# Optimization experiments

Measured on AMD Instinct MI355X. Metric: run time of the kernel, lower is better.

Reference implementation:

```python
import jax, jax.numpy as jnp
import numpy as np

B, T, D = 128, 512, 400
N_VALS, N_ACTS = 1024, 128

def setup_inputs() -> dict:
    key = jax.random.key(0)
    ks = jax.random.split(key, 7)
    H_utt = jax.random.normal(ks[0], (B, T, D), dtype=jnp.float32)
    c_utt = jax.random.normal(ks[1], (B, D), dtype=jnp.float32)
    C_acts = jax.random.normal(ks[2], (B, N_ACTS, D), dtype=jnp.float32)
    C_vals = jax.random.normal(ks[3], (N_VALS, 1, D), dtype=jnp.float32)
    W_score = jax.random.normal(ks[4], (1, D), dtype=jnp.float32) * (1.0 / np.sqrt(D))
    b_score = jnp.zeros((1,), dtype=jnp.float32)
    lens = jax.random.randint(ks[5], (B,), T // 2, T + 1, dtype=jnp.int64 if jax.config.read('jax_enable_x64') else jnp.int32)
    lens = lens.at[0].set(T)  # ensure max(lens) == T so masking matches torch semantics
    return {"H_utt": H_utt, "c_utt": c_utt, "C_acts": C_acts, "C_vals": C_vals,
            "W_score": W_score, "b_score": b_score, "utterance_len": lens}

def reference(H_utt, c_utt, C_acts, C_vals, W_score, b_score, utterance_len):
    vals = C_vals[:, 0, :]                                   # [V, D]
    # --- y_utts: default attention of each value vector over utterance states ---
    scores = jnp.einsum('btd,vd->bvt', H_utt, vals)          # mul+sum scoring
    mask = jnp.arange(T)[None, :] < utterance_len[:, None]   # [B, T]
    scores = jnp.where(mask[:, None, :], scores, -jnp.inf)
    probs = jax.nn.softmax(scores, axis=-1)                  # [B, V, T]
    q_utts = jnp.einsum('bvt,btd->bvd', probs, H_utt)        # weighted sum contexts
    y_utts = jnp.einsum('bvd,d->bv', q_utts, W_score[0]) + b_score[0]  # utt_scorer
    # --- y_acts: attention of c_utt over per-example act vectors, then score vs vals ---
    s2 = jnp.einsum('bad,bd->ba', C_acts, c_utt)
    p2 = jax.nn.softmax(s2, axis=-1)
    q_acts = jnp.einsum('ba,bad->bd', p2, C_acts)            # [B, D]
    y_acts = q_acts @ vals.T                                 # [B, V]
    return (y_utts, y_acts)
```

## Files before the change

### kernel.cpp

```cpp
#include <hip/hip_runtime.h>
#include <hip/hip_bf16.h>

#define B_  128
#define T_  512
#define D_  400
#define NV  1024
#define NA  128

#define LDH  424
#define NT   32
#define MV   128
#define MAIN_BLOCKS 1024

typedef __bf16 bf16_t;
typedef bf16_t bf16x8 __attribute__((ext_vector_type(8)));
typedef bf16_t bf16x4 __attribute__((ext_vector_type(4)));
typedef float  floatx4 __attribute__((ext_vector_type(4)));

__device__ inline void async_copy16(const void* g, void* l) {
    __builtin_amdgcn_global_load_lds(
        (const __attribute__((address_space(1))) unsigned int*)g,
        (__attribute__((address_space(3))) unsigned int*)l, 16, 0, 0);
}

__device__ inline float dot4(float4 a, float4 b) {
    return a.x * b.x + a.y * b.y + a.z * b.z + a.w * b.w;
}

__global__ __launch_bounds__(256) void prep_kernel(const float* __restrict__ H,
                                                   const float* __restrict__ W,
                                                   const float* __restrict__ Ca,
                                                   const float* __restrict__ cu,
                                                   float* __restrict__ hw,
                                                   bf16_t* __restrict__ Hbf,
                                                   float* __restrict__ s2) {
    int wave = threadIdx.x >> 6;
    int lane = threadIdx.x & 63;
    if (blockIdx.x < B_ * T_ / 4) {
        long row = (long)blockIdx.x * 4 + wave;
        const float* h = H + row * D_;
        bf16_t* orow = Hbf + row * (long)LDH;
        float acc = 0.f;
        if (lane < 50) {
            const float4* p  = (const float4*)(h + lane * 8);
            const float4* wp = (const float4*)(W + lane * 8);
            float4 x = p[0], y = p[1];
            acc = dot4(x, wp[0]) + dot4(y, wp[1]);
            bf16x8 f;
            f[0] = (bf16_t)x.x; f[1] = (bf16_t)x.y; f[2] = (bf16_t)x.z; f[3] = (bf16_t)x.w;
            f[4] = (bf16_t)y.x; f[5] = (bf16_t)y.y; f[6] = (bf16_t)y.z; f[7] = (bf16_t)y.w;
            *(bf16x8*)(orow + lane * 8) = f;
        } else if (lane < 53) {
            bf16x8 z;
#pragma unroll
            for (int j = 0; j < 8; ++j) z[j] = (bf16_t)0.0f;
            *(bf16x8*)(orow + 400 + (lane - 50) * 8) = z;
        }
#pragma unroll
        for (int off = 1; off < 64; off <<= 1) acc += __shfl_xor(acc, off, 64);
        if (lane == 0) hw[row] = acc;
    } else {
        long row = (long)(blockIdx.x - B_ * T_ / 4) * 4 + wave;
        int b = (int)(row >> 7);
        const float4* a4 = (const float4*)(Ca + row * (long)D_);
        const float4* c4 = (const float4*)(cu + (long)b * D_);
        float acc = dot4(a4[lane], c4[lane]);
        if (lane < 36) acc += dot4(a4[lane + 64], c4[lane + 64]);
#pragma unroll
        for (int off = 1; off < 64; off <<= 1) acc += __shfl_xor(acc, off, 64);
        if (lane == 0) s2[row] = acc;
    }
}

__global__ __launch_bounds__(256) void prep_nb_kernel(const float* __restrict__ H,
                                                      const float* __restrict__ W,
                                                      const float* __restrict__ Ca,
                                                      const float* __restrict__ cu,
                                                      float* __restrict__ hw,
                                                      float* __restrict__ s2) {
    int wave = threadIdx.x >> 6;
    int lane = threadIdx.x & 63;
    if (blockIdx.x < B_ * T_ / 4) {
        long row = (long)blockIdx.x * 4 + wave;
        const float* h = H + row * D_;
        float acc = 0.f;
        for (int k = lane; k < D_; k += 64) acc += h[k] * W[k];
#pragma unroll
        for (int off = 1; off < 64; off <<= 1) acc += __shfl_xor(acc, off, 64);
        if (lane == 0) hw[row] = acc;
    } else {
        long row = (long)(blockIdx.x - B_ * T_ / 4) * 4 + wave;
        int b = (int)(row >> 7);
        const float4* a4 = (const float4*)(Ca + row * (long)D_);
        const float4* c4 = (const float4*)(cu + (long)b * D_);
        float acc = dot4(a4[lane], c4[lane]);
        if (lane < 36) acc += dot4(a4[lane + 64], c4[lane + 64]);
#pragma unroll
        for (int off = 1; off < 64; off <<= 1) acc += __shfl_xor(acc, off, 64);
        if (lane == 0) s2[row] = acc;
    }
}

__global__ __launch_bounds__(256) void qacts_kernel(const float* __restrict__ s2,
                                                    const float* __restrict__ Ca,
                                                    float* __restrict__ q_ws) {
    __shared__ float p_lds[NA];
    __shared__ float red[8];
    __shared__ __align__(16) float4 part[100];
    int b = blockIdx.x;
    int tid = threadIdx.x, wave = tid >> 6, lane = tid & 63;

    float s = (tid < NA) ? s2[(long)b * NA + tid] : -3.0e38f;
    float m = s;
#pragma unroll
    for (int off = 1; off < 64; off <<= 1) m = fmaxf(m, __shfl_xor(m, off, 64));
    if (lane == 0) red[wave] = m;
    __syncthreads();
    m = fmaxf(red[0], red[1]);
    float e = (tid < NA) ? __expf(s - m) : 0.f;
    float sum = e;
#pragma unroll
    for (int off = 1; off < 64; off <<= 1) sum += __shfl_xor(sum, off, 64);
    if (lane == 0) red[4 + wave] = sum;
    __syncthreads();
    float S = red[4] + red[5];
    if (tid < NA) p_lds[tid] = e / S;
    __syncthreads();

    int c4 = tid % 100;
    int half = tid / 100;
    float4 acc0 = {0.f, 0.f, 0.f, 0.f};
    if (tid < 200) {
        const float4* Cb4 = (const float4*)(Ca + (size_t)b * NA * D_);
        float4 acc1 = {0.f, 0.f, 0.f, 0.f};
        int a0 = half * 64;
#pragma unroll 4
        for (int a = 0; a < 64; a += 2) {
            float p0 = p_lds[a0 + a], p1 = p_lds[a0 + a + 1];
            float4 x0 = Cb4[(size_t)(a0 + a) * 100 + c4];
            float4 x1 = Cb4[(size_t)(a0 + a + 1) * 100 + c4];
            acc0.x += p0 * x0.x; acc0.y += p0 * x0.y; acc0.z += p0 * x0.z; acc0.w += p0 * x0.w;
            acc1.x += p1 * x1.x; acc1.y += p1 * x1.y; acc1.z += p1 * x1.z; acc1.w += p1 * x1.w;
        }
        acc0.x += acc1.x; acc0.y += acc1.y; acc0.z += acc1.z; acc0.w += acc1.w;
        if (half == 1) part[c4] = acc0;
    }
    __syncthreads();
    if (tid < 100) {
        float4 o = part[c4];
        o.x += acc0.x; o.y += acc0.y; o.z += acc0.z; o.w += acc0.w;
        ((float4*)(q_ws + (size_t)b * D_))[c4] = o;
    }
}

template<int PRE>
__global__ __launch_bounds__(256, 3) void main_kernel(const float* __restrict__ H,
                                                      const bf16_t* __restrict__ Hbf,
                                                      const float* __restrict__ Cv,
                                                      const float* __restrict__ hw,
                                                      const float* __restrict__ bs,
                                                      const int* __restrict__ lens,
                                                      const float* __restrict__ q_ws,
                                                      float* __restrict__ out) {
    __shared__ bf16_t h_lds[NT * LDH + 256];
    __shared__ float hw_lds[NT];

    int tid = threadIdx.x;
    int wave = tid >> 6, lane = tid & 63;

    if (blockIdx.x >= MAIN_BLOCKS) {
        long grp = (long)(blockIdx.x - MAIN_BLOCKS) * 4 + wave;
        int b = (int)(grp >> 8);
        int v0 = (int)(grp & 255) * 4;
        const float4* q4 = (const float4*)(q_ws + (size_t)b * D_);
        float4 qa = q4[lane];
        float4 qb = (lane < 36) ? q4[lane + 64] : make_float4(0.f, 0.f, 0.f, 0.f);
        float acc[4];
#pragma unroll
        for (int r = 0; r < 4; ++r) {
            const float4* v4 = (const float4*)(Cv + (size_t)(v0 + r) * D_);
            acc[r] = dot4(v4[lane], qa);
            if (lane < 36) acc[r] += dot4(v4[lane + 64], qb);
        }
#pragma unroll
        for (int off = 1; off < 64; off <<= 1) {
#pragma unroll
            for (int r = 0; r < 4; ++r) acc[r] += __shfl_xor(acc[r], off, 64);
        }
        if (lane == 0) {
            float4 o = make_float4(acc[0], acc[1], acc[2], acc[3]);
            *(float4*)(out + (size_t)B_ * NV + (size_t)b * NV + v0) = o;
        }
        return;
    }

    int i = blockIdx.x;
    int xcd = i & 7, vc = (i >> 3) & 7, bb = i >> 6;
    int b = xcd + 8 * bb;
    int vbase = vc * MV;

    int lrow = lane & 15, quad = lane >> 4;
    int len = lens[b];
    float b0 = bs[0];

    if (!PRE) {
        for (int idx = tid; idx < NT * (LDH - D_); idx += 256) {
            int r = idx / (LDH - D_), c = idx % (LDH - D_);
            h_lds[r * LDH + D_ + c] = (bf16_t)0.0f;
        }
    }

    bf16x8 afrag[2][13];
#pragma unroll
    for (int set = 0; set < 2; ++set) {
        const float* vrow = Cv + (size_t)(vbase + wave * 32 + set * 16 + lrow) * D_;
#pragma unroll
        for (int kk = 0; kk < 13; ++kk) {
            int k0 = kk * 32 + quad * 8;
            bf16x8 f;
            if (k0 >= D_) {
#pragma unroll
                for (int j = 0; j < 8; ++j) f[j] = (bf16_t)0.0f;
            } else {
                const float4* p = (const float4*)(vrow + k0);
                float4 x = p[0], y = p[1];
                f[0] = (bf16_t)x.x; f[1] = (bf16_t)x.y;
                f[2] = (bf16_t)x.z; f[3] = (bf16_t)x.w;
                f[4] = (bf16_t)y.x; f[5] = (bf16_t)y.y;
                f[6] = (bf16_t)y.z; f[7] = (bf16_t)y.w;
            }
            afrag[set][kk] = f;
        }
    }

    float m_s = -3.0e38f;
    float l_s[2][4], a_s[2][4];
#pragma unroll
    for (int set = 0; set < 2; ++set)
#pragma unroll
        for (int r = 0; r < 4; ++r) { l_s[set][r] = 0.f; a_s[set][r] = 0.f; }

    int ntiles = (len + NT - 1) / NT;
    const float* Hb = H + (size_t)b * T_ * D_;
    const bf16_t* Hbfb = Hbf + (size_t)b * T_ * LDH;

    for (int tt = 0; tt < ntiles; ++tt) {
        int t0 = tt * NT;
        __syncthreads();
        if (PRE) {
            const char* gt = (const char*)(Hbfb + (size_t)t0 * LDH);
            char* lt = (char*)h_lds;
#pragma unroll 1
            for (int c = wave; c < 27; c += 4)
                async_copy16(gt + c * 1024 + lane * 16, lt + c * 1024 + lane * 16);
        } else {
            for (int idx = tid; idx < NT * (D_ / 4); idx += 256) {
                int r = idx / (D_ / 4), c4 = idx % (D_ / 4);
                float4 x = *(const float4*)(Hb + (size_t)(t0 + r) * D_ + c4 * 4);
                bf16x4 f;
                f[0] = (bf16_t)x.x; f[1] = (bf16_t)x.y;
                f[2] = (bf16_t)x.z; f[3] = (bf16_t)x.w;
                *(bf16x4*)(&h_lds[r * LDH + c4 * 4]) = f;
            }
        }
        if (tid < NT) hw_lds[tid] = hw[(size_t)b * T_ + t0 + tid];
        __syncthreads();

        floatx4 c[2][2];
        floatx4 zero4 = {0.f, 0.f, 0.f, 0.f};
#pragma unroll
        for (int set = 0; set < 2; ++set)
#pragma unroll
            for (int s = 0; s < 2; ++s) c[set][s] = zero4;

#pragma unroll
        for (int kk = 0; kk < 13; ++kk) {
            int koff = kk * 32 + quad * 8;
#pragma unroll
            for (int s = 0; s < 2; ++s) {
                bf16x8 bfr = *(const bf16x8*)(&h_lds[(s * 16 + lrow) * LDH + koff]);
                c[0][s] = __builtin_amdgcn_mfma_f32_16x16x32_bf16(afrag[0][kk], bfr, c[0][s], 0, 0, 0);
                c[1][s] = __builtin_amdgcn_mfma_f32_16x16x32_bf16(afrag[1][kk], bfr, c[1][s], 0, 0, 0);
            }
        }

        if (t0 + NT > len) {
#pragma unroll
            for (int s = 0; s < 2; ++s) {
                int t = t0 + s * 16 + lrow;
                if (t >= len) {
#pragma unroll
                    for (int set = 0; set < 2; ++set) {
                        c[set][s][0] = -3.0e38f; c[set][s][1] = -3.0e38f;
                        c[set][s][2] = -3.0e38f; c[set][s][3] = -3.0e38f;
                    }
                }
            }
        }

        float hw0 = hw_lds[lrow], hw1 = hw_lds[16 + lrow];

        float cm = fmaxf(fmaxf(fmaxf(c[0][0][0], c[0][0][1]), fmaxf(c[0][0][2], c[0][0][3])),
                         fmaxf(fmaxf(c[0][1][0], c[0][1][1]), fmaxf(c[0][1][2], c[0][1][3])));
        cm = fmaxf(cm,
             fmaxf(fmaxf(fmaxf(c[1][0][0], c[1][0][1]), fmaxf(c[1][0][2], c[1][0][3])),
                   fmaxf(fmaxf(c[1][1][0], c[1][1][1]), fmaxf(c[1][1][2], c[1][1][3]))));
        float mn = fmaxf(m_s, cm);
        float alpha = __expf(m_s - mn);
        m_s = mn;
#pragma unroll
        for (int set = 0; set < 2; ++set)
#pragma unroll
            for (int r = 0; r < 4; ++r) {
                float p0 = __expf(c[set][0][r] - mn);
                float p1 = __expf(c[set][1][r] - mn);
                l_s[set][r] = l_s[set][r] * alpha + (p0 + p1);
                a_s[set][r] = a_s[set][r] * alpha + (p0 * hw0 + p1 * hw1);
            }
    }

#pragma unroll
    for (int set = 0; set < 2; ++set)
#pragma unroll
        for (int r = 0; r < 4; ++r) {
            float m = m_s, l = l_s[set][r], a = a_s[set][r];
#pragma unroll
            for (int off = 1; off < 16; off <<= 1) {
                float mo = __shfl_xor(m, off, 64);
                float lo = __shfl_xor(l, off, 64);
                float ao = __shfl_xor(a, off, 64);
                float mx = fmaxf(m, mo);
                float f1 = __expf(m - mx), f2 = __expf(mo - mx);
                l = l * f1 + lo * f2;
                a = a * f1 + ao * f2;
                m = mx;
            }
            if (lrow == 0) {
                int v = vbase + wave * 32 + set * 16 + quad * 4 + r;
                out[(size_t)b * NV + v] = a / l + b0;
            }
        }
}

extern "C" void kernel_launch(void* const* d_in, const int* in_sizes, int n_in,
                              void* d_out, int out_size, void* d_ws, size_t ws_size,
                              hipStream_t stream) {
    const float* H    = (const float*)d_in[0];
    const float* cu   = (const float*)d_in[1];
    const float* Ca   = (const float*)d_in[2];
    const float* Cv   = (const float*)d_in[3];
    const float* W    = (const float*)d_in[4];
    const float* bs   = (const float*)d_in[5];
    const int*   lens = (const int*)d_in[6];
    float* out = (float*)d_out;

    float*  hw   = (float*)d_ws;
    float*  q_ws = hw + (size_t)B_ * T_;
    float*  s2   = q_ws + (size_t)B_ * D_;
    bf16_t* Hbf  = (bf16_t*)(s2 + (size_t)B_ * NA);

    size_t need = ((size_t)B_ * T_ + (size_t)B_ * D_ + (size_t)B_ * NA) * sizeof(float)
                + (size_t)B_ * T_ * LDH * sizeof(bf16_t)
                + 4096;
    bool pre = (ws_size >= need);

    int prep_blocks = B_ * T_ / 4 + B_ * NA / 4;
    if (pre) {
        prep_kernel<<<dim3(prep_blocks), dim3(256), 0, stream>>>(H, W, Ca, cu, hw, Hbf, s2);
    } else {
        prep_nb_kernel<<<dim3(prep_blocks), dim3(256), 0, stream>>>(H, W, Ca, cu, hw, s2);
    }
    qacts_kernel<<<dim3(B_), dim3(256), 0, stream>>>(s2, Ca, q_ws);
    int fused_blocks = MAIN_BLOCKS + B_ * NV / 16;
    if (pre) {
        main_kernel<1><<<dim3(fused_blocks), dim3(256), 0, stream>>>(H, Hbf, Cv, hw, bs, lens, q_ws, out);
    } else {
        main_kernel<0><<<dim3(fused_blocks), dim3(256), 0, stream>>>(H, Hbf, Cv, hw, bs, lens, q_ws, out);
    }
}
```

Measured before the change: 288.5 us.

## Pre-swizzle H into MFMA fragment layout and stream from registers, dropping LDS

The prep kernel now writes H as bf16 in 16-row tiles already arranged in the MFMA B-fragment order, so each lane loads its fragment straight from global memory with no LDS staging and no block barriers. The main kernel gives each wave 64 values (four 16-wide sets) and double-buffers tile fragments in registers, with half as many blocks at occupancy 1. Padded tiles past the length are skipped at 16-row granularity. This removes the LDS round trip and syncthreads, but register pressure is higher, occupancy is lower, and every wave rereads the H tiles from global/L2.

```diff
diff --git a/kernel.cpp b/kernel.cpp
--- a/kernel.cpp
+++ b/kernel.cpp
@@ -7,21 +7,17 @@
 #define NV  1024
 #define NA  128
 
+#define TILE_BYTES 13312
+#define MAIN_BLOCKS 512
+
 #define LDH  424
 #define NT   32
-#define MV   128
-#define MAIN_BLOCKS 1024
+#define FB_MAIN_BLOCKS 1024
 
 typedef __bf16 bf16_t;
 typedef bf16_t bf16x8 __attribute__((ext_vector_type(8)));
 typedef bf16_t bf16x4 __attribute__((ext_vector_type(4)));
 typedef float  floatx4 __attribute__((ext_vector_type(4)));
-
-__device__ inline void async_copy16(const void* g, void* l) {
-    __builtin_amdgcn_global_load_lds(
-        (const __attribute__((address_space(1))) unsigned int*)g,
-        (__attribute__((address_space(3))) unsigned int*)l, 16, 0, 0);
-}
 
 __device__ inline float dot4(float4 a, float4 b) {
     return a.x * b.x + a.y * b.y + a.z * b.z + a.w * b.w;
@@ -32,64 +28,40 @@
                                                    const float* __restrict__ Ca,
                                                    const float* __restrict__ cu,
                                                    float* __restrict__ hw,
-                                                   bf16_t* __restrict__ Hbf,
+                                                   bf16_t* __restrict__ Hf,
                                                    float* __restrict__ s2) {
     int wave = threadIdx.x >> 6;
     int lane = threadIdx.x & 63;
-    if (blockIdx.x < B_ * T_ / 4) {
-        long row = (long)blockIdx.x * 4 + wave;
-        const float* h = H + row * D_;
-        bf16_t* orow = Hbf + row * (long)LDH;
+    if (blockIdx.x < 1024) {
+        int tile = blockIdx.x * 4 + wave;
+        int b = tile >> 5, ti = tile & 31;
+        int lrow = lane & 15, quad = lane >> 4;
+        const float* hrow = H + ((size_t)b * T_ + ti * 16 + lrow) * D_;
+        char* fdst = (char*)Hf + (size_t)tile * TILE_BYTES + lane * 16;
         float acc = 0.f;
-        if (lane < 50) {
-            const float4* p  = (const float4*)(h + lane * 8);
-            const float4* wp = (const float4*)(W + lane * 8);
-            float4 x = p[0], y = p[1];
-            acc = dot4(x, wp[0]) + dot4(y, wp[1]);
+#pragma unroll
+        for (int kk = 0; kk < 13; ++kk) {
+            int k0 = kk * 32 + quad * 8;
             bf16x8 f;
-            f[0] = (bf16_t)x.x; f[1] = (bf16_t)x.y; f[2] = (bf16_t)x.z; f[3] = (bf16_t)x.w;
-            f[4] = (bf16_t)y.x; f[5] = (bf16_t)y.y; f[6] = (bf16_t)y.z; f[7] = (bf16_t)y.w;
-            *(bf16x8*)(orow + lane * 8) = f;
-        } else if (lane < 53) {
-            bf16x8 z;
-#pragma unroll
-            for (int j = 0; j < 8; ++j) z[j] = (bf16_t)0.0f;
-            *(bf16x8*)(orow + 400 + (lane - 50) * 8) = z;
-        }
-#pragma unroll
-        for (int off = 1; off < 64; off <<= 1) acc += __shfl_xor(acc, off, 64);
-        if (lane == 0) hw[row] = acc;
+            if (k0 < D_) {
+                float4 x = *(const float4*)(hrow + k0);
+                float4 y = *(const float4*)(hrow + k0 + 4);
+                float4 wx = *(const float4*)(W + k0);
+                float4 wy = *(const float4*)(W + k0 + 4);
+                acc += dot4(x, wx) + dot4(y, wy);
+                f[0] = (bf16_t)x.x; f[1] = (bf16_t)x.y; f[2] = (bf16_t)x.z; f[3] = (bf16_t)x.w;
+                f[4] = (bf16_t)y.x; f[5] = (bf16_t)y.y; f[6] = (bf16_t)y.z; f[7] = (bf16_t)y.w;
+            } else {
+#pragma unroll
+                for (int j = 0; j < 8; ++j) f[j] = (bf16_t)0.0f;
+            }
+            *(bf16x8*)(fdst + kk * 1024) = f;
+        }
+        acc += __shfl_xor(acc, 16, 64);
+        acc += __shfl_xor(acc, 32, 64);
+        if (lane < 16) hw[b * T_ + ti * 16 + lane] = acc;
     } else {
-        long row = (long)(blockIdx.x - B_ * T_ / 4) * 4 + wave;
-        int b = (int)(row >> 7);
-        const float4* a4 = (const float4*)(Ca + row * (long)D_);
-        const float4* c4 = (const float4*)(cu + (long)b * D_);
-        float acc = dot4(a4[lane], c4[lane]);
-        if (lane < 36) acc += dot4(a4[lane + 64], c4[lane + 64]);
-#pragma unroll
-        for (int off = 1; off < 64; off <<= 1) acc += __shfl_xor(acc, off, 64);
-        if (lane == 0) s2[row] = acc;
-    }
-}
-
-__global__ __launch_bounds__(256) void prep_nb_kernel(const float* __restrict__ H,
-                                                      const float* __restrict__ W,
-                                                      const float* __restrict__ Ca,
-                                                      const float* __restrict__ cu,
-                                                      float* __restrict__ hw,
-                                                      float* __restrict__ s2) {
-    int wave = threadIdx.x >> 6;
-    int lane = threadIdx.x & 63;
-    if (blockIdx.x < B_ * T_ / 4) {
-        long row = (long)blockIdx.x * 4 + wave;
-        const float* h = H + row * D_;
-        float acc = 0.f;
-        for (int k = lane; k < D_; k += 64) acc += h[k] * W[k];
-#pragma unroll
-        for (int off = 1; off < 64; off <<= 1) acc += __shfl_xor(acc, off, 64);
-        if (lane == 0) hw[row] = acc;
-    } else {
-        long row = (long)(blockIdx.x - B_ * T_ / 4) * 4 + wave;
+        long row = (long)(blockIdx.x - 1024) * 4 + wave;
         int b = (int)(row >> 7);
         const float4* a4 = (const float4*)(Ca + row * (long)D_);
         const float4* c4 = (const float4*)(cu + (long)b * D_);
@@ -153,18 +125,48 @@
     }
 }
 
-template<int PRE>
-__global__ __launch_bounds__(256, 3) void main_kernel(const float* __restrict__ H,
-                                                      const bf16_t* __restrict__ Hbf,
+#define LDTILE(BUF, TI)                                                        \
+    _Pragma("unroll") for (int kk = 0; kk < 13; ++kk)                          \
+        BUF[kk] = *(const bf16x8*)(fb + (size_t)(TI) * TILE_BYTES + kk * 1024);
+
+#define COMPUTE(BUF, TI)                                                       \
+    do {                                                                       \
+        floatx4 c_[4];                                                         \
+        _Pragma("unroll") for (int s_ = 0; s_ < 4; ++s_) c_[s_] = zero4;       \
+        _Pragma("unroll") for (int kk = 0; kk < 13; ++kk) {                    \
+            bf16x8 bb_ = BUF[kk];                                              \
+            _Pragma("unroll") for (int s_ = 0; s_ < 4; ++s_)                   \
+                c_[s_] = __builtin_amdgcn_mfma_f32_16x16x32_bf16(              \
+                    afrag[s_][kk], bb_, c_[s_], 0, 0, 0);                      \
+        }                                                                      \
+        int t_ = (TI) * 16 + lrow;                                             \
+        float hwv_ = hwb[t_];                                                  \
+        bool ok_ = t_ < len;                                                   \
+        float cm_ = -3.0e38f;                                                  \
+        _Pragma("unroll") for (int s_ = 0; s_ < 4; ++s_)                       \
+            _Pragma("unroll") for (int r_ = 0; r_ < 4; ++r_) {                 \
+                float v_ = ok_ ? c_[s_][r_] : -3.0e38f;                        \
+                c_[s_][r_] = v_;                                               \
+                cm_ = fmaxf(cm_, v_);                                          \
+            }                                                                  \
+        float mn_ = fmaxf(m_s, cm_);                                           \
+        float alpha_ = __expf(m_s - mn_);                                      \
+        m_s = mn_;                                                             \
+        _Pragma("unroll") for (int s_ = 0; s_ < 4; ++s_)                       \
+            _Pragma("unroll") for (int r_ = 0; r_ < 4; ++r_) {                 \
+                float p_ = __expf(c_[s_][r_] - mn_);                           \
+                l_s[s_][r_] = l_s[s_][r_] * alpha_ + p_;                       \
+                a_s[s_][r_] = a_s[s_][r_] * alpha_ + p_ * hwv_;                \
+            }                                                                  \
+    } while (0)
+
+__global__ __launch_bounds__(256, 1) void main_kernel(const bf16_t* __restrict__ Hf,
                                                       const float* __restrict__ Cv,
                                                       const float* __restrict__ hw,
                                                       const float* __restrict__ bs,
                                                       const int* __restrict__ lens,
                                                       const float* __restrict__ q_ws,
                                                       float* __restrict__ out) {
-    __shared__ bf16_t h_lds[NT * LDH + 256];
-    __shared__ float hw_lds[NT];
-
     int tid = threadIdx.x;
     int wave = tid >> 6, lane = tid & 63;
 
@@ -195,25 +197,18 @@
     }
 
     int i = blockIdx.x;
-    int xcd = i & 7, vc = (i >> 3) & 7, bb = i >> 6;
+    int xcd = i & 7, vc = (i >> 3) & 3, bb = i >> 5;
     int b = xcd + 8 * bb;
-    int vbase = vc * MV;
+    int vbase = vc * 256 + wave * 64;
 
     int lrow = lane & 15, quad = lane >> 4;
     int len = lens[b];
     float b0 = bs[0];
 
-    if (!PRE) {
-        for (int idx = tid; idx < NT * (LDH - D_); idx += 256) {
-            int r = idx / (LDH - D_), c = idx % (LDH - D_);
-            h_lds[r * LDH + D_ + c] = (bf16_t)0.0f;
-        }
-    }
-
-    bf16x8 afrag[2][13];
-#pragma unroll
-    for (int set = 0; set < 2; ++set) {
-        const float* vrow = Cv + (size_t)(vbase + wave * 32 + set * 16 + lrow) * D_;
+    bf16x8 afrag[4][13];
+#pragma unroll
+    for (int set = 0; set < 4; ++set) {
+        const float* vrow = Cv + (size_t)(vbase + set * 16 + lrow) * D_;
 #pragma unroll
         for (int kk = 0; kk < 13; ++kk) {
             int k0 = kk * 32 + quad * 8;
@@ -234,6 +229,159 @@
     }
 
     float m_s = -3.0e38f;
+    float l_s[4][4], a_s[4][4];
+#pragma unroll
+    for (int s = 0; s < 4; ++s)
+#pragma unroll
+        for (int r = 0; r < 4; ++r) { l_s[s][r] = 0.f; a_s[s][r] = 0.f; }
+
+    const floatx4 zero4 = {0.f, 0.f, 0.f, 0.f};
+    const float* hwb = hw + (size_t)b * T_;
+    const char* fb = (const char*)Hf + (size_t)b * 32 * TILE_BYTES + lane * 16;
+
+    int ntiles = (len + 15) >> 4;
+    bf16x8 bfA[13], bfB[13];
+
+    LDTILE(bfA, 0);
+    int ti = 0;
+    while (true) {
+        if (ti + 1 < ntiles) { LDTILE(bfB, ti + 1); }
+        COMPUTE(bfA, ti);
+        ++ti; if (ti == ntiles) break;
+        if (ti + 1 < ntiles) { LDTILE(bfA, ti + 1); }
+        COMPUTE(bfB, ti);
+        ++ti; if (ti == ntiles) break;
+    }
+
+#pragma unroll
+    for (int s = 0; s < 4; ++s)
+#pragma unroll
+        for (int r = 0; r < 4; ++r) {
+            float m = m_s, l = l_s[s][r], a = a_s[s][r];
+#pragma unroll
+            for (int off = 1; off < 16; off <<= 1) {
+                float mo = __shfl_xor(m, off, 64);
+                float lo = __shfl_xor(l, off, 64);
+                float ao = __shfl_xor(a, off, 64);
+                float mx = fmaxf(m, mo);
+                float f1 = __expf(m - mx), f2 = __expf(mo - mx);
+                l = l * f1 + lo * f2;
+                a = a * f1 + ao * f2;
+                m = mx;
+            }
+            if (lrow == 0) {
+                int v = vbase + s * 16 + quad * 4 + r;
+                out[(size_t)b * NV + v] = a / l + b0;
+            }
+        }
+}
+
+__global__ __launch_bounds__(256) void prep_fb_kernel(const float* __restrict__ H,
+                                                      const float* __restrict__ W,
+                                                      const float* __restrict__ Ca,
+                                                      const float* __restrict__ cu,
+                                                      float* __restrict__ hw,
+                                                      float* __restrict__ s2) {
+    int wave = threadIdx.x >> 6;
+    int lane = threadIdx.x & 63;
+    if (blockIdx.x < B_ * T_ / 4) {
+        long row = (long)blockIdx.x * 4 + wave;
+        const float* h = H + row * D_;
+        float acc = 0.f;
+        for (int k = lane; k < D_; k += 64) acc += h[k] * W[k];
+#pragma unroll
+        for (int off = 1; off < 64; off <<= 1) acc += __shfl_xor(acc, off, 64);
+        if (lane == 0) hw[row] = acc;
+    } else {
+        long row = (long)(blockIdx.x - B_ * T_ / 4) * 4 + wave;
+        int b = (int)(row >> 7);
+        const float4* a4 = (const float4*)(Ca + row * (long)D_);
+        const float4* c4 = (const float4*)(cu + (long)b * D_);
+        float acc = dot4(a4[lane], c4[lane]);
+        if (lane < 36) acc += dot4(a4[lane + 64], c4[lane + 64]);
+#pragma unroll
+        for (int off = 1; off < 64; off <<= 1) acc += __shfl_xor(acc, off, 64);
+        if (lane == 0) s2[row] = acc;
+    }
+}
+
+__global__ __launch_bounds__(256, 2) void main_fb_kernel(const float* __restrict__ H,
+                                                         const float* __restrict__ Cv,
+                                                         const float* __restrict__ hw,
+                                                         const float* __restrict__ bs,
+                                                         const int* __restrict__ lens,
+                                                         const float* __restrict__ q_ws,
+                                                         float* __restrict__ out) {
+    __shared__ bf16_t h_lds[NT * LDH];
+    __shared__ float hw_lds[NT];
+
+    int tid = threadIdx.x;
+    int wave = tid >> 6, lane = tid & 63;
+
+    if (blockIdx.x >= FB_MAIN_BLOCKS) {
+        long grp = (long)(blockIdx.x - FB_MAIN_BLOCKS) * 4 + wave;
+        int b = (int)(grp >> 8);
+        int v0 = (int)(grp & 255) * 4;
+        const float4* q4 = (const float4*)(q_ws + (size_t)b * D_);
+        float4 qa = q4[lane];
+        float4 qb = (lane < 36) ? q4[lane + 64] : make_float4(0.f, 0.f, 0.f, 0.f);
+        float acc[4];
+#pragma unroll
+        for (int r = 0; r < 4; ++r) {
+            const float4* v4 = (const float4*)(Cv + (size_t)(v0 + r) * D_);
+            acc[r] = dot4(v4[lane], qa);
+            if (lane < 36) acc[r] += dot4(v4[lane + 64], qb);
+        }
+#pragma unroll
+        for (int off = 1; off < 64; off <<= 1) {
+#pragma unroll
+            for (int r = 0; r < 4; ++r) acc[r] += __shfl_xor(acc[r], off, 64);
+        }
+        if (lane == 0) {
+            float4 o = make_float4(acc[0], acc[1], acc[2], acc[3]);
+            *(float4*)(out + (size_t)B_ * NV + (size_t)b * NV + v0) = o;
+        }
+        return;
+    }
+
+    int i = blockIdx.x;
+    int xcd = i & 7, vc = (i >> 3) & 7, bb = i >> 6;
+    int b = xcd + 8 * bb;
+    int vbase = vc * 128;
+
+    int lrow = lane & 15, quad = lane >> 4;
+    int len = lens[b];
+    float b0 = bs[0];
+
+    for (int idx = tid; idx < NT * (LDH - D_); idx += 256) {
+        int r = idx / (LDH - D_), c = idx % (LDH - D_);
+        h_lds[r * LDH + D_ + c] = (bf16_t)0.0f;
+    }
+
+    bf16x8 afrag[2][13];
+#pragma unroll
+    for (int set = 0; set < 2; ++set) {
+        const float* vrow = Cv + (size_t)(vbase + wave * 32 + set * 16 + lrow) * D_;
+#pragma unroll
+        for (int kk = 0; kk < 13; ++kk) {
+            int k0 = kk * 32 + quad * 8;
+            bf16x8 f;
+            if (k0 >= D_) {
+#pragma unroll
+                for (int j = 0; j < 8; ++j) f[j] = (bf16_t)0.0f;
+            } else {
+                const float4* p = (const float4*)(vrow + k0);
+                float4 x = p[0], y = p[1];
+                f[0] = (bf16_t)x.x; f[1] = (bf16_t)x.y;
+                f[2] = (bf16_t)x.z; f[3] = (bf16_t)x.w;
+                f[4] = (bf16_t)y.x; f[5] = (bf16_t)y.y;
+                f[6] = (bf16_t)y.z; f[7] = (bf16_t)y.w;
+            }
+            afrag[set][kk] = f;
+        }
+    }
+
+    float m_s = -3.0e38f;
     float l_s[2][4], a_s[2][4];
 #pragma unroll
     for (int set = 0; set < 2; ++set)
@@ -242,26 +390,17 @@
 
     int ntiles = (len + NT - 1) / NT;
     const float* Hb = H + (size_t)b * T_ * D_;
-    const bf16_t* Hbfb = Hbf + (size_t)b * T_ * LDH;
 
     for (int tt = 0; tt < ntiles; ++tt) {
         int t0 = tt * NT;
         __syncthreads();
-        if (PRE) {
-            const char* gt = (const char*)(Hbfb + (size_t)t0 * LDH);
-            char* lt = (char*)h_lds;
-#pragma unroll 1
-            for (int c = wave; c < 27; c += 4)
-                async_copy16(gt + c * 1024 + lane * 16, lt + c * 1024 + lane * 16);
-        } else {
-            for (int idx = tid; idx < NT * (D_ / 4); idx += 256) {
-                int r = idx / (D_ / 4), c4 = idx % (D_ / 4);
-                float4 x = *(const float4*)(Hb + (size_t)(t0 + r) * D_ + c4 * 4);
-                bf16x4 f;
-                f[0] = (bf16_t)x.x; f[1] = (bf16_t)x.y;
-                f[2] = (bf16_t)x.z; f[3] = (bf16_t)x.w;
-                *(bf16x4*)(&h_lds[r * LDH + c4 * 4]) = f;
-            }
+        for (int idx = tid; idx < NT * (D_ / 4); idx += 256) {
+            int r = idx / (D_ / 4), c4 = idx % (D_ / 4);
+            float4 x = *(const float4*)(Hb + (size_t)(t0 + r) * D_ + c4 * 4);
+            bf16x4 f;
+            f[0] = (bf16_t)x.x; f[1] = (bf16_t)x.y;
+            f[2] = (bf16_t)x.z; f[3] = (bf16_t)x.w;
+            *(bf16x4*)(&h_lds[r * LDH + c4 * 4]) = f;
         }
         if (tid < NT) hw_lds[tid] = hw[(size_t)b * T_ + t0 + tid];
         __syncthreads();
@@ -299,12 +438,13 @@
         }
 
         float hw0 = hw_lds[lrow], hw1 = hw_lds[16 + lrow];
-
-        float cm = fmaxf(fmaxf(fmaxf(c[0][0][0], c[0][0][1]), fmaxf(c[0][0][2], c[0][0][3])),
-                         fmaxf(fmaxf(c[0][1][0], c[0][1][1]), fmaxf(c[0][1][2], c[0][1][3])));
-        cm = fmaxf(cm,
-             fmaxf(fmaxf(fmaxf(c[1][0][0], c[1][0][1]), fmaxf(c[1][0][2], c[1][0][3])),
-                   fmaxf(fmaxf(c[1][1][0], c[1][1][1]), fmaxf(c[1][1][2], c[1][1][3]))));
+        float cm = -3.0e38f;
+#pragma unroll
+        for (int set = 0; set < 2; ++set)
+#pragma unroll
+            for (int s = 0; s < 2; ++s)
+#pragma unroll
+                for (int r = 0; r < 4; ++r) cm = fmaxf(cm, c[set][s][r]);
         float mn = fmaxf(m_s, cm);
         float alpha = __expf(m_s - mn);
         m_s = mn;
@@ -357,24 +497,19 @@
     float*  hw   = (float*)d_ws;
     float*  q_ws = hw + (size_t)B_ * T_;
     float*  s2   = q_ws + (size_t)B_ * D_;
-    bf16_t* Hbf  = (bf16_t*)(s2 + (size_t)B_ * NA);
+    bf16_t* Hf   = (bf16_t*)(s2 + (size_t)B_ * NA);
 
     size_t need = ((size_t)B_ * T_ + (size_t)B_ * D_ + (size_t)B_ * NA) * sizeof(float)
-                + (size_t)B_ * T_ * LDH * sizeof(bf16_t)
-                + 4096;
+                + (size_t)4096 * TILE_BYTES;
     bool pre = (ws_size >= need);
 
-    int prep_blocks = B_ * T_ / 4 + B_ * NA / 4;
     if (pre) {
-        prep_kernel<<<dim3(prep_blocks), dim3(256), 0, stream>>>(H, W, Ca, cu, hw, Hbf, s2);
+        prep_kernel<<<dim3(1024 + B_ * NA / 4), dim3(256), 0, stream>>>(H, W, Ca, cu, hw, Hf, s2);
+        qacts_kernel<<<dim3(B_), dim3(256), 0, stream>>>(s2, Ca, q_ws);
+        main_kernel<<<dim3(MAIN_BLOCKS + B_ * NV / 16), dim3(256), 0, stream>>>(Hf, Cv, hw, bs, lens, q_ws, out);
     } else {
-        prep_nb_kernel<<<dim3(prep_blocks), dim3(256), 0, stream>>>(H, W, Ca, cu, hw, s2);
-    }
-    qacts_kernel<<<dim3(B_), dim3(256), 0, stream>>>(s2, Ca, q_ws);
-    int fused_blocks = MAIN_BLOCKS + B_ * NV / 16;
-    if (pre) {
-        main_kernel<1><<<dim3(fused_blocks), dim3(256), 0, stream>>>(H, Hbf, Cv, hw, bs, lens, q_ws, out);
-    } else {
-        main_kernel<0><<<dim3(fused_blocks), dim3(256), 0, stream>>>(H, Hbf, Cv, hw, bs, lens, q_ws, out);
-    }
-}
+        prep_fb_kernel<<<dim3(B_ * T_ / 4 + B_ * NA / 4), dim3(256), 0, stream>>>(H, W, Ca, cu, hw, s2);
+        qacts_kernel<<<dim3(B_), dim3(256), 0, stream>>>(s2, Ca, q_ws);
+        main_fb_kernel<<<dim3(FB_MAIN_BLOCKS + B_ * NV / 16), dim3(256), 0, stream>>>(H, Cv, hw, bs, lens, q_ws, out);
+    }
+}
```

New measurement: 314.4 us. 1.09x slower.
